# Performance work log

Hardware: AMD Instinct MI355X
Metric: run time of the kernel (lower is better)

## Reference

```python
import jax, jax.numpy as jnp
import numpy as np

NEG = -1e30  # mask value safe for logsumexp/max
HALF_POS = 4   # positive window: [t-4, t+4)
HALF_ALL = 16  # combined window: [t-16, t+16) (pos + 12 negatives each side)


def _normalize(x, axis=-1, eps=1e-12):
    # matches torch F.normalize: x / max(||x||, eps)
    n = jnp.linalg.norm(x, axis=axis, keepdims=True)
    return x / jnp.maximum(n, eps)


def _banded_logits(q, k, temperature):
    # q, k: [B, T, D] (normalized). Returns logits [B, T, W], valid mask, pos mask.
    B, T, D = q.shape
    offsets = jnp.arange(-HALF_ALL, HALF_ALL)          # [W=32]
    j = jnp.arange(T)[:, None] + offsets[None, :]      # [T, W] absolute indices
    valid = (j >= 0) & (j < T)                         # combined (pos+neg) window
    jc = jnp.clip(j, 0, T - 1)
    kg = k[:, jc, :]                                   # [B, T, W, D]
    logits = jnp.einsum('btd,btwd->btw', q, kg) / temperature
    pos = valid & (offsets >= -HALF_POS)[None, :] & (offsets < HALF_POS)[None, :]
    return logits, valid, pos


def _direction(q, k, temperature):
    logits, valid, pos = _banded_logits(q, k, temperature)
    lse_all = jax.nn.logsumexp(jnp.where(valid, logits, NEG), axis=2)  # [B, T]
    lse_pos = jax.nn.logsumexp(jnp.where(pos, logits, NEG), axis=2)    # [B, T]
    # per-t loss is mean over batch; summed over t
    loss_sum = jnp.sum(jnp.mean(lse_all - lse_pos, axis=0))
    max_all = jnp.max(jnp.where(valid, logits, NEG), axis=2)
    max_pos = jnp.max(jnp.where(pos, logits, NEG), axis=2)
    # argmax falls in positive block (positives listed first -> ties go positive)
    correct = jnp.sum((max_pos >= max_all).astype(jnp.float32))
    return loss_sum, correct


def setup_inputs() -> dict:
    key = jax.random.key(0)
    k1, k2 = jax.random.split(key)
    B, T, D = 16, 4096, 128
    return {
        'motion_feature': jax.random.normal(k1, (B, T, D), dtype=jnp.float32),
        'audio_feature': jax.random.normal(k2, (B, T, D), dtype=jnp.float32),
    }


def reference(motion_feature, audio_feature):
    temperature = 0.1
    B, T, D = motion_feature.shape
    m = _normalize(motion_feature, axis=2)
    a = _normalize(audio_feature, axis=2)
    m2a_loss, m2a_correct = _direction(m, a, temperature)
    a2m_loss, a2m_correct = _direction(a, m, temperature)
    final_loss = (m2a_loss + a2m_loss) / (2 * T)
    total_correct = (m2a_correct + a2m_correct) / (2 * T * B)
    return final_loss, total_correct
```

## Files before the change

### kernel.cpp

```cpp
#include <hip/hip_runtime.h>
#include <hip/hip_bf16.h>

typedef __attribute__((ext_vector_type(8))) short bf16x8;
typedef __attribute__((ext_vector_type(4))) float f32x4;

#define T_DIM 4096
#define B_DIM 16
#define D_DIM 128
#define TILE 64
#define NTILE 4
#define ROWS 96
#define SROW 136
#define TBUF (ROWS * SROW)
#define NEGV -1e30f
#define NBLK 256
#define SCALE (1.0f / 131072.0f)

#define LDS_BARRIER() asm volatile("s_waitcnt lgkmcnt(0)\n\ts_barrier" ::: "memory")

__global__ __launch_bounds__(512, 2) void lcl_main(
    const float* __restrict__ mot, const float* __restrict__ aud,
    float* __restrict__ ws)
{
    __shared__ unsigned short sbuf[2 * 2 * TBUF];
    __shared__ float redL[8], redC[8];

    const int tid  = threadIdx.x;
    const int lane = tid & 63;
    const int wv   = tid >> 6;
    const int g32  = tid >> 5;
    const int l32  = tid & 31;

    const int lin = blockIdx.x;
    const int swz = (lin & 7) * (NBLK / 8) + (lin >> 3);
    const int by  = swz >> 4;
    const int tg  = swz & 15;
    const int tbase = tg * (NTILE * TILE);
    const size_t base = (size_t)by * (T_DIM * D_DIM);
    const bool edge = (tg == 0) || (tg == 15);

    const int dir = wv >> 2;
    const int mi  = wv & 3;

    const int fr    = lane & 15;
    const int fch   = (lane >> 4) * 8;
    const int col16 = lane & 15;
    const int g     = lane >> 4;

    float4 vm[6], va[6];
    auto issue = [&](int tstart) {
        const size_t off = base + (size_t)(tstart - 16 + g32) * D_DIM + l32 * 4;
        const float* spm = mot + off;
        const float* spa = aud + off;
        if (!edge) {
            #pragma unroll
            for (int i = 0; i < 6; ++i) {
                vm[i] = *reinterpret_cast<const float4*>(spm + (size_t)(16 * i) * D_DIM);
                va[i] = *reinterpret_cast<const float4*>(spa + (size_t)(16 * i) * D_DIM);
            }
        } else {
            #pragma unroll
            for (int i = 0; i < 6; ++i) {
                const bool ok = (unsigned)(tstart - 16 + g32 + 16 * i) < (unsigned)T_DIM;
                vm[i] = make_float4(0.f, 0.f, 0.f, 0.f);
                va[i] = vm[i];
                if (ok) {
                    vm[i] = *reinterpret_cast<const float4*>(spm + (size_t)(16 * i) * D_DIM);
                    va[i] = *reinterpret_cast<const float4*>(spa + (size_t)(16 * i) * D_DIM);
                }
            }
        }
    };

    issue(tbase);

    float lossW = 0.f, corrW = 0.f;

    #pragma unroll
    for (int tile = 0; tile < NTILE; ++tile) {
        const int t0  = tbase + tile * TILE;
        const int cur = tile & 1;
        unsigned short* smc = sbuf + (cur * 2 + 0) * TBUF;
        unsigned short* sac = sbuf + (cur * 2 + 1) * TBUF;

        {
            unsigned short* dpm = smc + g32 * SROW + l32 * 4;
            unsigned short* dpa = sac + g32 * SROW + l32 * 4;
            #pragma unroll
            for (int i = 0; i < 6; ++i) {
                union { __hip_bfloat16 h[4]; uint2 u; } pm, pa;
                pm.h[0] = __float2bfloat16(vm[i].x);
                pm.h[1] = __float2bfloat16(vm[i].y);
                pm.h[2] = __float2bfloat16(vm[i].z);
                pm.h[3] = __float2bfloat16(vm[i].w);
                pa.h[0] = __float2bfloat16(va[i].x);
                pa.h[1] = __float2bfloat16(va[i].y);
                pa.h[2] = __float2bfloat16(va[i].z);
                pa.h[3] = __float2bfloat16(va[i].w);
                *reinterpret_cast<uint2*>(dpm + 16 * i * SROW) = pm.u;
                *reinterpret_cast<uint2*>(dpa + 16 * i * SROW) = pa.u;
            }
        }

        if (tile + 1 < NTILE) issue(t0 + TILE);

        LDS_BARRIER();

        const unsigned short* q = (dir ? sac : smc);
        const unsigned short* k = (dir ? smc : sac);
        f32x4 acc0 = {0.f,0.f,0.f,0.f}, acc1 = acc0, acc2 = acc0;
        f32x4 n0 = acc0, n1 = acc0, n2 = acc0, nq = acc0;
        const unsigned short* qrow = q + (16 * (mi + 1) + fr) * SROW + fch;
        const unsigned short* k0   = k + ((mi + 0) * 16 + fr) * SROW + fch;
        const unsigned short* k1   = k + ((mi + 1) * 16 + fr) * SROW + fch;
        const unsigned short* k2   = k + ((mi + 2) * 16 + fr) * SROW + fch;
        #pragma unroll
        for (int ks = 0; ks < 4; ++ks) {
            bf16x8 bq = *reinterpret_cast<const bf16x8*>(qrow + ks * 32);
            bf16x8 a0 = *reinterpret_cast<const bf16x8*>(k0   + ks * 32);
            bf16x8 a1 = *reinterpret_cast<const bf16x8*>(k1   + ks * 32);
            bf16x8 a2 = *reinterpret_cast<const bf16x8*>(k2   + ks * 32);
            acc0 = __builtin_amdgcn_mfma_f32_16x16x32_bf16(a0, bq, acc0, 0, 0, 0);
            acc1 = __builtin_amdgcn_mfma_f32_16x16x32_bf16(a1, bq, acc1, 0, 0, 0);
            acc2 = __builtin_amdgcn_mfma_f32_16x16x32_bf16(a2, bq, acc2, 0, 0, 0);
            n0   = __builtin_amdgcn_mfma_f32_16x16x32_bf16(a0, a0, n0, 0, 0, 0);
            n1   = __builtin_amdgcn_mfma_f32_16x16x32_bf16(a1, a1, n1, 0, 0, 0);
            n2   = __builtin_amdgcn_mfma_f32_16x16x32_bf16(a2, a2, n2, 0, 0, 0);
            nq   = __builtin_amdgcn_mfma_f32_16x16x32_bf16(bq, bq, nq, 0, 0, 0);
        }

        const int rs = col16 & 3;
        const float dq = (rs == 0) ? nq[0] : (rs == 1) ? nq[1] : (rs == 2) ? nq[2] : nq[3];
        const float d0 = (rs == 0) ? n0[0] : (rs == 1) ? n0[1] : (rs == 2) ? n0[2] : n0[3];
        const float d1 = (rs == 0) ? n1[0] : (rs == 1) ? n1[1] : (rs == 2) ? n1[2] : n1[3];
        const float d2 = (rs == 0) ? n2[0] : (rs == 1) ? n2[1] : (rs == 2) ? n2[2] : n2[3];
        const float iq = rsqrtf(fmaxf(dq, 1e-24f));
        const float i0 = rsqrtf(fmaxf(d0, 1e-24f));
        const float i1 = rsqrtf(fmaxf(d1, 1e-24f));
        const float i2 = rsqrtf(fmaxf(d2, 1e-24f));

        const float scq10 = 10.0f * __shfl(iq, col16 + 16 * (col16 >> 2));
        const int srcn = 20 * g;
        f32x4 sck0, sck1, sck2;
        #pragma unroll
        for (int r = 0; r < 4; ++r) {
            sck0[r] = __shfl(i0, srcn + r);
            sck1[r] = __shfl(i1, srcn + r);
            sck2[r] = __shfl(i2, srcn + r);
        }

        const int jbase  = t0 - 16 + 16 * mi + 4 * g;
        const int kkbase = 4 * g - col16;

        float lv[12];
        bool  pmk[12];
        float mx = NEGV, mxp = NEGV;
        #pragma unroll
        for (int bb = 0; bb < 3; ++bb) {
            const f32x4 acc = (bb == 0) ? acc0 : ((bb == 1) ? acc1 : acc2);
            const f32x4 sck = (bb == 0) ? sck0 : ((bb == 1) ? sck1 : sck2);
            #pragma unroll
            for (int r = 0; r < 4; ++r) {
                const int kk = kkbase + 16 * bb + r;
                const int jg = jbase  + 16 * bb + r;
                const bool ok = ((unsigned)kk < 32u) && ((unsigned)jg < (unsigned)T_DIM);
                const float li = ok ? acc[r] * (scq10 * sck[r]) : NEGV;
                const bool  pi = ((unsigned)(kk - 12) < 8u);
                lv[bb * 4 + r]  = li;
                pmk[bb * 4 + r] = pi;
                mx  = fmaxf(mx, li);
                mxp = pi ? fmaxf(mxp, li) : mxp;
            }
        }
        mx  = fmaxf(mx,  __shfl_xor(mx,  16));
        mx  = fmaxf(mx,  __shfl_xor(mx,  32));
        mxp = fmaxf(mxp, __shfl_xor(mxp, 16));
        mxp = fmaxf(mxp, __shfl_xor(mxp, 32));

        float s = 0.f, sp = 0.f;
        #pragma unroll
        for (int i = 0; i < 12; ++i) {
            const float e = __expf(lv[i] - mx);
            s  += e;
            sp += pmk[i] ? e : 0.f;
        }
        s  += __shfl_xor(s,  16);  s  += __shfl_xor(s,  32);
        sp += __shfl_xor(sp, 16);  sp += __shfl_xor(sp, 32);

        if (g == 0) {
            lossW += __logf(s / sp);
            corrW += (mxp >= mx) ? 1.0f : 0.0f;
        }
    }

    #pragma unroll
    for (int m = 32; m; m >>= 1) {
        lossW += __shfl_xor(lossW, m);
        corrW += __shfl_xor(corrW, m);
    }
    if (lane == 0) { redL[wv] = lossW; redC[wv] = corrW; }
    __syncthreads();
    if (tid == 0) {
        float L = 0.f, C = 0.f;
        #pragma unroll
        for (int i = 0; i < 8; ++i) { L += redL[i]; C += redC[i]; }
        ws[2 * swz]     = L;
        ws[2 * swz + 1] = C;
    }
}

__global__ __launch_bounds__(256) void lcl_final(
    const float* __restrict__ ws, float* __restrict__ out)
{
    const int tid = threadIdx.x;
    const float2 v = reinterpret_cast<const float2*>(ws)[tid];
    float L = v.x, C = v.y;
    #pragma unroll
    for (int m = 32; m; m >>= 1) { L += __shfl_xor(L, m); C += __shfl_xor(C, m); }
    __shared__ float rl[4], rc[4];
    if ((tid & 63) == 0) { rl[tid >> 6] = L; rc[tid >> 6] = C; }
    __syncthreads();
    if (tid == 0) {
        out[0] = (rl[0] + rl[1] + rl[2] + rl[3]) * SCALE;
        out[1] = (rc[0] + rc[1] + rc[2] + rc[3]) * SCALE;
    }
}

extern "C" void kernel_launch(void* const* d_in, const int* in_sizes, int n_in,
                              void* d_out, int out_size, void* d_ws, size_t ws_size,
                              hipStream_t stream) {
    const float* mot = (const float*)d_in[0];
    const float* aud = (const float*)d_in[1];
    float* out = (float*)d_out;
    float* ws  = (float*)d_ws;

    lcl_main<<<NBLK, 512, 0, stream>>>(mot, aud, ws);
    lcl_final<<<1, 256, 0, stream>>>(ws, out);
}
```

Before: 21.44 us.

## Widen global loads and LDS stores, use exp2 softmax, single-wave final reduce

Each thread now loads 8 contiguous floats per row (two float4) and writes one 16-byte bf16 vector to LDS, replacing 4-float loads and 8-byte stores. The aim is fewer, wider memory instructions in the staging phase. The logits are pre-scaled by log2(e) so the softmax uses exp2f and log2f, avoiding an extra multiply per exponential. The final reduction kernel runs as a single 64-thread wave, removing the LDS round trip and the block barrier.

```diff
diff --git a/kernel.cpp b/kernel.cpp
--- a/kernel.cpp
+++ b/kernel.cpp
@@ -15,6 +15,8 @@
 #define NEGV -1e30f
 #define NBLK 256
 #define SCALE (1.0f / 131072.0f)
+#define LOG2E 1.4426950408889634f
+#define LN2   0.6931471805599453f
 
 #define LDS_BARRIER() asm volatile("s_waitcnt lgkmcnt(0)\n\ts_barrier" ::: "memory")
 
@@ -28,8 +30,8 @@
     const int tid  = threadIdx.x;
     const int lane = tid & 63;
     const int wv   = tid >> 6;
-    const int g32  = tid >> 5;
-    const int l32  = tid & 31;
+    const int r16b = tid >> 4;
+    const int l16  = tid & 15;
 
     const int lin = blockIdx.x;
     const int swz = (lin & 7) * (NBLK / 8) + (lin >> 3);
@@ -49,24 +51,32 @@
 
     float4 vm[6], va[6];
     auto issue = [&](int tstart) {
-        const size_t off = base + (size_t)(tstart - 16 + g32) * D_DIM + l32 * 4;
+        const size_t off = base + (size_t)(tstart - 16 + r16b) * D_DIM + l16 * 8;
         const float* spm = mot + off;
         const float* spa = aud + off;
         if (!edge) {
             #pragma unroll
-            for (int i = 0; i < 6; ++i) {
-                vm[i] = *reinterpret_cast<const float4*>(spm + (size_t)(16 * i) * D_DIM);
-                va[i] = *reinterpret_cast<const float4*>(spa + (size_t)(16 * i) * D_DIM);
+            for (int i = 0; i < 3; ++i) {
+                const float* pm_ = spm + (size_t)(32 * i) * D_DIM;
+                const float* pa_ = spa + (size_t)(32 * i) * D_DIM;
+                vm[2*i]   = *reinterpret_cast<const float4*>(pm_);
+                vm[2*i+1] = *reinterpret_cast<const float4*>(pm_ + 4);
+                va[2*i]   = *reinterpret_cast<const float4*>(pa_);
+                va[2*i+1] = *reinterpret_cast<const float4*>(pa_ + 4);
             }
         } else {
             #pragma unroll
-            for (int i = 0; i < 6; ++i) {
-                const bool ok = (unsigned)(tstart - 16 + g32 + 16 * i) < (unsigned)T_DIM;
-                vm[i] = make_float4(0.f, 0.f, 0.f, 0.f);
-                va[i] = vm[i];
+            for (int i = 0; i < 3; ++i) {
+                const bool ok = (unsigned)(tstart - 16 + r16b + 32 * i) < (unsigned)T_DIM;
+                vm[2*i] = make_float4(0.f, 0.f, 0.f, 0.f);
+                vm[2*i+1] = vm[2*i]; va[2*i] = vm[2*i]; va[2*i+1] = vm[2*i];
                 if (ok) {
-                    vm[i] = *reinterpret_cast<const float4*>(spm + (size_t)(16 * i) * D_DIM);
-                    va[i] = *reinterpret_cast<const float4*>(spa + (size_t)(16 * i) * D_DIM);
+                    const float* pm_ = spm + (size_t)(32 * i) * D_DIM;
+                    const float* pa_ = spa + (size_t)(32 * i) * D_DIM;
+                    vm[2*i]   = *reinterpret_cast<const float4*>(pm_);
+                    vm[2*i+1] = *reinterpret_cast<const float4*>(pm_ + 4);
+                    va[2*i]   = *reinterpret_cast<const float4*>(pa_);
+                    va[2*i+1] = *reinterpret_cast<const float4*>(pa_ + 4);
                 }
             }
         }
@@ -84,21 +94,29 @@
         unsigned short* sac = sbuf + (cur * 2 + 1) * TBUF;
 
         {
-            unsigned short* dpm = smc + g32 * SROW + l32 * 4;
-            unsigned short* dpa = sac + g32 * SROW + l32 * 4;
-            #pragma unroll
-            for (int i = 0; i < 6; ++i) {
-                union { __hip_bfloat16 h[4]; uint2 u; } pm, pa;
-                pm.h[0] = __float2bfloat16(vm[i].x);
-                pm.h[1] = __float2bfloat16(vm[i].y);
-                pm.h[2] = __float2bfloat16(vm[i].z);
-                pm.h[3] = __float2bfloat16(vm[i].w);
-                pa.h[0] = __float2bfloat16(va[i].x);
-                pa.h[1] = __float2bfloat16(va[i].y);
-                pa.h[2] = __float2bfloat16(va[i].z);
-                pa.h[3] = __float2bfloat16(va[i].w);
-                *reinterpret_cast<uint2*>(dpm + 16 * i * SROW) = pm.u;
-                *reinterpret_cast<uint2*>(dpa + 16 * i * SROW) = pa.u;
+            unsigned short* dpm = smc + r16b * SROW + l16 * 8;
+            unsigned short* dpa = sac + r16b * SROW + l16 * 8;
+            #pragma unroll
+            for (int i = 0; i < 3; ++i) {
+                union { __hip_bfloat16 h[8]; uint4 u; } pm_, pa_;
+                pm_.h[0] = __float2bfloat16(vm[2*i].x);
+                pm_.h[1] = __float2bfloat16(vm[2*i].y);
+                pm_.h[2] = __float2bfloat16(vm[2*i].z);
+                pm_.h[3] = __float2bfloat16(vm[2*i].w);
+                pm_.h[4] = __float2bfloat16(vm[2*i+1].x);
+                pm_.h[5] = __float2bfloat16(vm[2*i+1].y);
+                pm_.h[6] = __float2bfloat16(vm[2*i+1].z);
+                pm_.h[7] = __float2bfloat16(vm[2*i+1].w);
+                pa_.h[0] = __float2bfloat16(va[2*i].x);
+                pa_.h[1] = __float2bfloat16(va[2*i].y);
+                pa_.h[2] = __float2bfloat16(va[2*i].z);
+                pa_.h[3] = __float2bfloat16(va[2*i].w);
+                pa_.h[4] = __float2bfloat16(va[2*i+1].x);
+                pa_.h[5] = __float2bfloat16(va[2*i+1].y);
+                pa_.h[6] = __float2bfloat16(va[2*i+1].z);
+                pa_.h[7] = __float2bfloat16(va[2*i+1].w);
+                *reinterpret_cast<uint4*>(dpm + 32 * i * SROW) = pm_.u;
+                *reinterpret_cast<uint4*>(dpa + 32 * i * SROW) = pa_.u;
             }
         }
 
@@ -139,7 +157,7 @@
         const float i1 = rsqrtf(fmaxf(d1, 1e-24f));
         const float i2 = rsqrtf(fmaxf(d2, 1e-24f));
 
-        const float scq10 = 10.0f * __shfl(iq, col16 + 16 * (col16 >> 2));
+        const float scqL = (10.0f * LOG2E) * __shfl(iq, col16 + 16 * (col16 >> 2));
         const int srcn = 20 * g;
         f32x4 sck0, sck1, sck2;
         #pragma unroll
@@ -164,7 +182,7 @@
                 const int kk = kkbase + 16 * bb + r;
                 const int jg = jbase  + 16 * bb + r;
                 const bool ok = ((unsigned)kk < 32u) && ((unsigned)jg < (unsigned)T_DIM);
-                const float li = ok ? acc[r] * (scq10 * sck[r]) : NEGV;
+                const float li = ok ? acc[r] * (scqL * sck[r]) : NEGV;
                 const bool  pi = ((unsigned)(kk - 12) < 8u);
                 lv[bb * 4 + r]  = li;
                 pmk[bb * 4 + r] = pi;
@@ -180,7 +198,7 @@
         float s = 0.f, sp = 0.f;
         #pragma unroll
         for (int i = 0; i < 12; ++i) {
-            const float e = __expf(lv[i] - mx);
+            const float e = exp2f(lv[i] - mx);
             s  += e;
             sp += pmk[i] ? e : 0.f;
         }
@@ -188,7 +206,7 @@
         sp += __shfl_xor(sp, 16);  sp += __shfl_xor(sp, 32);
 
         if (g == 0) {
-            lossW += __logf(s / sp);
+            lossW += LN2 * __log2f(s / sp);
             corrW += (mxp >= mx) ? 1.0f : 0.0f;
         }
     }
@@ -209,20 +227,23 @@
     }
 }
 
-__global__ __launch_bounds__(256) void lcl_final(
+__global__ __launch_bounds__(64) void lcl_final(
     const float* __restrict__ ws, float* __restrict__ out)
 {
     const int tid = threadIdx.x;
-    const float2 v = reinterpret_cast<const float2*>(ws)[tid];
-    float L = v.x, C = v.y;
+    const float2* w2 = reinterpret_cast<const float2*>(ws);
+    float L = 0.f, C = 0.f;
+    #pragma unroll
+    for (int i = 0; i < 4; ++i) {
+        const float2 v = w2[tid + i * 64];
+        L += v.x;
+        C += v.y;
+    }
     #pragma unroll
     for (int m = 32; m; m >>= 1) { L += __shfl_xor(L, m); C += __shfl_xor(C, m); }
-    __shared__ float rl[4], rc[4];
-    if ((tid & 63) == 0) { rl[tid >> 6] = L; rc[tid >> 6] = C; }
-    __syncthreads();
     if (tid == 0) {
-        out[0] = (rl[0] + rl[1] + rl[2] + rl[3]) * SCALE;
-        out[1] = (rc[0] + rc[1] + rc[2] + rc[3]) * SCALE;
+        out[0] = L * SCALE;
+        out[1] = C * SCALE;
     }
 }
 
@@ -235,5 +256,5 @@
     float* ws  = (float*)d_ws;
 
     lcl_main<<<NBLK, 512, 0, stream>>>(mot, aud, ws);
-    lcl_final<<<1, 256, 0, stream>>>(ws, out);
+    lcl_final<<<1, 64, 0, stream>>>(ws, out);
 }
```

Result: no change. 21.50 us (+0.3%).
